# Kernel optimization log

Hardware: AMD Instinct MI355X
Metric: run time of the kernel (lower is better)

Reference implementation:

```python
import jax, jax.numpy as jnp
import numpy as np

COS_EPS = 1e-8
LN_EPS = 1e-5
N_HEADS = 8


def _merge(tokens, num_merge, wa, wb):
    """Faithful port of the torch merging loops.

    Torch computes topk(sim, num_merge) but the loop only reads indices[i,0]
    and indices[i,1] for i < num_merge, i.e. the top-2 per row -> we compute
    top_k(sim, 2) which yields identical values (modulo tie order).
    The per-step gather/average/scatter is sequential (later steps see earlier
    writes), so it is expressed as a lax.scan.
    """
    if num_merge == 0:
        return tokens
    n = jnp.linalg.norm(tokens, axis=-1)                      # [N]
    sim = (tokens @ tokens.T) / jnp.maximum(n[:, None] * n[None, :], COS_EPS)
    _, idx = jax.lax.top_k(sim, 2)                            # [N, 2]
    ab = idx[:num_merge]                                      # [num_merge, 2]

    def step(tok, ab_i):
        a, b = ab_i[0], ab_i[1]
        new = wa * tok[a] + wb * tok[b]
        # torch: tokens[a] = wa*tokens[a] + wb*tokens[b]; tokens[b] = tokens[a]
        return tok.at[a].set(new).at[b].set(new), None

    tokens, _ = jax.lax.scan(step, tokens, ab)
    return tokens[: tokens.shape[0] - num_merge]


def _layernorm(x, g, b):
    m = jnp.mean(x, axis=-1, keepdims=True)
    v = jnp.var(x, axis=-1, keepdims=True)
    return (x - m) * jax.lax.rsqrt(v + LN_EPS) * g + b


def _mha(x, Wqkv, bqkv, Wo, bo):
    """torch.nn.MultiheadAttention on an unbatched (L, D) input, q=k=v=x."""
    L, D = x.shape
    dh = D // N_HEADS
    qkv = x @ Wqkv.T + bqkv                                   # [L, 3D]
    q, k, v = jnp.split(qkv, 3, axis=-1)
    q = q.reshape(L, N_HEADS, dh)
    k = k.reshape(L, N_HEADS, dh)
    v = v.reshape(L, N_HEADS, dh)
    scores = jnp.einsum('qhd,khd->hqk', q, k) / np.float32(np.sqrt(dh))
    attn = jax.nn.softmax(scores, axis=-1)
    out = jnp.einsum('hqk,khd->qhd', attn, v).reshape(L, D)
    return out @ Wo.T + bo


def setup_inputs() -> dict:
    key = jax.random.key(0)
    ks = jax.random.split(key, 6)
    D = 768
    s = np.float32(0.02)
    return {
        'video_features': jax.random.normal(ks[0], (160, 50, D), jnp.float32),
        'Wqkv': jax.random.normal(ks[1], (3 * D, D), jnp.float32) * s,
        'bqkv': jnp.zeros((3 * D,), jnp.float32),
        'Wo': jax.random.normal(ks[2], (D, D), jnp.float32) * s,
        'bo': jnp.zeros((D,), jnp.float32),
        'ln1_g': jnp.ones((D,), jnp.float32),
        'ln1_b': jnp.zeros((D,), jnp.float32),
        'W1': jax.random.normal(ks[3], (4 * D, D), jnp.float32) * s,
        'b1': jnp.zeros((4 * D,), jnp.float32),
        'W2': jax.random.normal(ks[4], (D, 4 * D), jnp.float32) * s,
        'b2': jnp.zeros((D,), jnp.float32),
        'ln2_g': jnp.ones((D,), jnp.float32),
        'ln2_b': jnp.zeros((D,), jnp.float32),
    }


def reference(video_features, Wqkv, bqkv, Wo, bo, ln1_g, ln1_b,
              W1, b1, W2, b2, ln2_g, ln2_b):
    r = 0.5
    D = video_features.shape[-1]
    tokens = video_features.reshape(-1, D)                      # [8000, 768]
    tokens = _merge(tokens, int(tokens.shape[0] * r), 0.5, 0.5)       # img_me_block -> 4000
    tokens = _merge(tokens, int(tokens.shape[0] * r), 0.5, 0.5)       # cross_clip  -> 2000
    attn_out = _mha(tokens, Wqkv, bqkv, Wo, bo)
    tokens = _layernorm(tokens + attn_out, ln1_g, ln1_b)
    tokens = _merge(tokens, int(tokens.shape[0] * (r / 2)), 0.6, 0.4)  # intra_clip -> 1500
    ffn = jax.nn.gelu(tokens @ W1.T + b1, approximate=False) @ W2.T + b2
    return _layernorm(tokens + ffn, ln2_g, ln2_b)               # [1500, 768]
```

## Files before the change

### kernel.cpp

```cpp
#include <hip/hip_runtime.h>
#include <math.h>

#define D 768

__device__ __forceinline__ void dot4(float& acc, const float4& a, const float4& b) {
  acc += a.x * b.x; acc += a.y * b.y; acc += a.z * b.z; acc += a.w * b.w;
}

__global__ __launch_bounds__(256) void copy_f4(const float4* __restrict__ in,
                                               float4* __restrict__ out, int n) {
  int i = blockIdx.x * blockDim.x + threadIdx.x;
  if (i < n) out[i] = in[i];
}

__global__ __launch_bounds__(64) void norms_k(const float* __restrict__ tok,
                                              float* __restrict__ norms, int N) {
  int row = blockIdx.x;
  if (row >= N) return;
  const float* r = tok + (size_t)row * D;
  float s = 0.f;
  for (int k = threadIdx.x; k < D; k += 64) { float v = r[k]; s += v * v; }
#pragma unroll
  for (int off = 32; off > 0; off >>= 1) s += __shfl_down(s, off);
  if (threadIdx.x == 0) norms[row] = sqrtf(s);
}

__global__ __launch_bounds__(256) void sim_top2_v2(
    const float* __restrict__ tok, const float* __restrict__ norms,
    int nRows, int nCols, int nChunks, float4* __restrict__ part) {
  __shared__ float As[64][36];
  __shared__ float Bs[64][36];
  __shared__ float Ss[64][68];
  int tid = threadIdx.x;
  int rowBase = blockIdx.y * 64, colBase = blockIdx.x * 64;
  int tx = tid & 15, ty = tid >> 4;
  float acc[4][4] = {};
  int sr = tid >> 3, sc = (tid & 7) * 4;
  for (int kb = 0; kb < D; kb += 32) {
#pragma unroll
    for (int p = 0; p < 2; p++) {
      int r = sr + 32 * p;
      int ga = rowBase + r;
      float4 v = (ga < nRows) ? *(const float4*)&tok[(size_t)ga * D + kb + sc]
                              : make_float4(0.f, 0.f, 0.f, 0.f);
      *(float4*)&As[r][sc] = v;
      int gb = colBase + r;
      float4 w = (gb < nCols) ? *(const float4*)&tok[(size_t)gb * D + kb + sc]
                              : make_float4(0.f, 0.f, 0.f, 0.f);
      *(float4*)&Bs[r][sc] = w;
    }
    __syncthreads();
#pragma unroll
    for (int d = 0; d < 32; d += 4) {
      float4 a0 = *(float4*)&As[ty][d];
      float4 a1 = *(float4*)&As[ty + 16][d];
      float4 a2 = *(float4*)&As[ty + 32][d];
      float4 a3 = *(float4*)&As[ty + 48][d];
      float4 b0 = *(float4*)&Bs[tx][d];
      float4 b1 = *(float4*)&Bs[tx + 16][d];
      float4 b2 = *(float4*)&Bs[tx + 32][d];
      float4 b3 = *(float4*)&Bs[tx + 48][d];
      dot4(acc[0][0], a0, b0); dot4(acc[0][1], a0, b1); dot4(acc[0][2], a0, b2); dot4(acc[0][3], a0, b3);
      dot4(acc[1][0], a1, b0); dot4(acc[1][1], a1, b1); dot4(acc[1][2], a1, b2); dot4(acc[1][3], a1, b3);
      dot4(acc[2][0], a2, b0); dot4(acc[2][1], a2, b1); dot4(acc[2][2], a2, b2); dot4(acc[2][3], a2, b3);
      dot4(acc[3][0], a3, b0); dot4(acc[3][1], a3, b1); dot4(acc[3][2], a3, b2); dot4(acc[3][3], a3, b3);
    }
    __syncthreads();
  }
  float na[4], nc[4];
#pragma unroll
  for (int i = 0; i < 4; i++) { int r = rowBase + ty + 16 * i; na[i] = (r < nRows) ? norms[r] : 1.f; }
#pragma unroll
  for (int j = 0; j < 4; j++) { int c = colBase + tx + 16 * j; nc[j] = (c < nCols) ? norms[c] : 1.f; }
#pragma unroll
  for (int i = 0; i < 4; i++)
#pragma unroll
    for (int j = 0; j < 4; j++) {
      int c = colBase + tx + 16 * j;
      Ss[ty + 16 * i][tx + 16 * j] =
          (c < nCols) ? acc[i][j] / fmaxf(na[i] * nc[j], 1e-8f) : -INFINITY;
    }
  __syncthreads();
  if (tid < 64) {
    int row = rowBase + tid;
    if (row < nRows) {
      float v1 = -INFINITY, v2 = -INFINITY;
      int i1 = -1, i2 = -1;
      for (int c = 0; c < 64; c++) {
        float v = Ss[tid][c];
        int id = colBase + c;
        if (v > v1) { v2 = v1; i2 = i1; v1 = v; i1 = id; }
        else if (v > v2) { v2 = v; i2 = id; }
      }
      part[(size_t)row * nChunks + blockIdx.x] =
          make_float4(v1, __int_as_float(i1), v2, __int_as_float(i2));
    }
  }
}

__global__ __launch_bounds__(256) void top2_reduce(const float4* __restrict__ part,
                                                   int nRows, int nChunks,
                                                   int2* __restrict__ pairs) {
  int row = blockIdx.x * 256 + threadIdx.x;
  if (row >= nRows) return;
  float v1 = -INFINITY, v2 = -INFINITY;
  int i1 = -1, i2 = -1;
  for (int c = 0; c < nChunks; c++) {
    float4 p = part[(size_t)row * nChunks + c];
    float v = p.x; int id = __float_as_int(p.y);
    if (id >= 0) {
      if (v > v1) { v2 = v1; i2 = i1; v1 = v; i1 = id; }
      else if (v > v2) { v2 = v; i2 = id; }
    }
    v = p.z; id = __float_as_int(p.w);
    if (id >= 0) {
      if (v > v1) { v2 = v1; i2 = i1; v1 = v; i1 = id; }
      else if (v > v2) { v2 = v; i2 = id; }
    }
  }
  pairs[row] = make_int2(i1, i2);
}

#define MSG 8
__global__ __launch_bounds__(64) void merge_scan5(float* __restrict__ tok,
                                                  const int2* __restrict__ pairs,
                                                  int nm, float wa, float wb) {
  __shared__ int2 sp[4000];
  int t = blockIdx.x * 64 + threadIdx.x;
  for (int i = threadIdx.x; i < nm; i += 64) sp[i] = pairs[i];
  __syncthreads();
  int s = 0;
  for (; s + MSG <= nm; s += MSG) {
    int aa[MSG], bb[MSG];
    float xx[MSG], yy[MSG], vv[MSG];
#pragma unroll
    for (int c = 0; c < MSG; c++) {
      int2 p = sp[s + c]; aa[c] = p.x; bb[c] = p.y;
    }
#pragma unroll
    for (int c = 0; c < MSG; c++) {
      xx[c] = tok[(size_t)aa[c] * D + t];
      yy[c] = tok[(size_t)bb[c] * D + t];
    }
#pragma unroll
    for (int c = 0; c < MSG; c++) {
      float xv = xx[c], yv = yy[c];
#pragma unroll
      for (int j = 0; j < c; j++) {
        bool fa = (aa[c] == aa[j]) || (aa[c] == bb[j]);
        bool fb = (bb[c] == aa[j]) || (bb[c] == bb[j]);
        xv = fa ? vv[j] : xv;
        yv = fb ? vv[j] : yv;
      }
      vv[c] = wa * xv + wb * yv;
    }
#pragma unroll
    for (int c = 0; c < MSG; c++) {
      bool la = true, lb = true;
#pragma unroll
      for (int j = c + 1; j < MSG; j++) {
        la = la && (aa[j] != aa[c]) && (bb[j] != aa[c]);
        lb = lb && (aa[j] != bb[c]) && (bb[j] != bb[c]);
      }
      if (la) tok[(size_t)aa[c] * D + t] = vv[c];
      if (lb) tok[(size_t)bb[c] * D + t] = vv[c];
    }
  }
  for (; s < nm; s++) {
    int2 p = sp[s];
    float x = tok[(size_t)p.x * D + t];
    float y = tok[(size_t)p.y * D + t];
    float v = wa * x + wb * y;
    tok[(size_t)p.x * D + t] = v;
    tok[(size_t)p.y * D + t] = v;
  }
}

__global__ __launch_bounds__(256) void gemm_nt_v2(const float* __restrict__ A,
                                                  const float* __restrict__ B,
                                                  const float* __restrict__ bias,
                                                  float* __restrict__ C,
                                                  int M, int N, int K, int act) {
  __shared__ float As[64][36];
  __shared__ float Bs[64][36];
  int tid = threadIdx.x;
  int rowBase = blockIdx.y * 64, colBase = blockIdx.x * 64;
  int tx = tid & 15, ty = tid >> 4;
  float acc[4][4] = {};
  int sr = tid >> 3, sc = (tid & 7) * 4;
  for (int kb = 0; kb < K; kb += 32) {
#pragma unroll
    for (int p = 0; p < 2; p++) {
      int r = sr + 32 * p;
      int ga = rowBase + r;
      float4 v = (ga < M) ? *(const float4*)&A[(size_t)ga * K + kb + sc]
                          : make_float4(0.f, 0.f, 0.f, 0.f);
      *(float4*)&As[r][sc] = v;
      int gb = colBase + r;
      float4 w = (gb < N) ? *(const float4*)&B[(size_t)gb * K + kb + sc]
                          : make_float4(0.f, 0.f, 0.f, 0.f);
      *(float4*)&Bs[r][sc] = w;
    }
    __syncthreads();
#pragma unroll
    for (int d = 0; d < 32; d += 4) {
      float4 a0 = *(float4*)&As[ty][d];
      float4 a1 = *(float4*)&As[ty + 16][d];
      float4 a2 = *(float4*)&As[ty + 32][d];
      float4 a3 = *(float4*)&As[ty + 48][d];
      float4 b0 = *(float4*)&Bs[tx][d];
      float4 b1 = *(float4*)&Bs[tx + 16][d];
      float4 b2 = *(float4*)&Bs[tx + 32][d];
      float4 b3 = *(float4*)&Bs[tx + 48][d];
      dot4(acc[0][0], a0, b0); dot4(acc[0][1], a0, b1); dot4(acc[0][2], a0, b2); dot4(acc[0][3], a0, b3);
      dot4(acc[1][0], a1, b0); dot4(acc[1][1], a1, b1); dot4(acc[1][2], a1, b2); dot4(acc[1][3], a1, b3);
      dot4(acc[2][0], a2, b0); dot4(acc[2][1], a2, b1); dot4(acc[2][2], a2, b2); dot4(acc[2][3], a2, b3);
      dot4(acc[3][0], a3, b0); dot4(acc[3][1], a3, b1); dot4(acc[3][2], a3, b2); dot4(acc[3][3], a3, b3);
    }
    __syncthreads();
  }
#pragma unroll
  for (int i = 0; i < 4; i++)
#pragma unroll
    for (int j = 0; j < 4; j++) {
      int row = rowBase + ty + 16 * i, col = colBase + tx + 16 * j;
      if (row < M && col < N) {
        float v = acc[i][j] + bias[col];
        if (act == 1) v = 0.5f * v * (1.0f + erff(v * 0.70710678118654752f));
        C[(size_t)row * N + col] = v;
      }
    }
}

#define QT5 16
__global__ __launch_bounds__(512) void attn_k5(const float* __restrict__ qkv,
                                               float* __restrict__ attnb, int L) {
  int h = blockIdx.y;
  int q0 = blockIdx.x * QT5;
  __shared__ float qs[QT5][100];
  __shared__ float ks[64][100];
  __shared__ float vs[64][100];
  __shared__ float ss[QT5][68];
  __shared__ float mrow[QT5], lrow[QT5], corr[QT5];
  int tid = threadIdx.x;
  const float scale = 0.10206207261596577f;
  if (tid < QT5 * 24) {
    int i = tid / 24, c4 = (tid % 24) * 4;
    int qr = q0 + i;
    float4 v = (qr < L) ? *(const float4*)&qkv[(size_t)qr * 2304 + h * 96 + c4]
                        : make_float4(0.f, 0.f, 0.f, 0.f);
    *(float4*)&qs[i][c4] = v;
  }
  if (tid < QT5) { mrow[tid] = -INFINITY; lrow[tid] = 0.f; }
  int pi = tid / 24, gpd = tid % 24;
  bool pvact = tid < QT5 * 24;
  float oa0 = 0.f, oa1 = 0.f, oa2 = 0.f, oa3 = 0.f;
  __syncthreads();
  for (int c0 = 0; c0 < L; c0 += 64) {
    int cn = min(64, L - c0);
    for (int p = tid; p < 64 * 24; p += 512) {
      int r = p / 24, gc = p % 24;
      int pc = 4 * (gc ^ ((r >> 3) & 3));
      bool ok = r < cn;
      float4 kv4 = ok ? *(const float4*)&qkv[(size_t)(c0 + r) * 2304 + 768 + h * 96 + gc * 4]
                      : make_float4(0.f, 0.f, 0.f, 0.f);
      *(float4*)&ks[r][pc] = kv4;
      float4 vv4 = ok ? *(const float4*)&qkv[(size_t)(c0 + r) * 2304 + 1536 + h * 96 + gc * 4]
                      : make_float4(0.f, 0.f, 0.f, 0.f);
      *(float4*)&vs[r][pc] = vv4;
    }
    __syncthreads();
    {
      int qi = tid >> 5;
      int m = tid & 31;
      int swzm = (m >> 3) & 3;
      float a0 = 0.f, a1 = 0.f;
#pragma unroll
      for (int gd = 0; gd < 24; gd++) {
        float4 q4 = *(float4*)&qs[qi][4 * gd];
        int pc = 4 * (gd ^ swzm);
        float4 k0 = *(float4*)&ks[m][pc];
        float4 k1 = *(float4*)&ks[m + 32][pc];
        dot4(a0, q4, k0);
        dot4(a1, q4, k1);
      }
      ss[qi][m] = a0 * scale;
      ss[qi][m + 32] = a1 * scale;
    }
    __syncthreads();
    if (tid < QT5) {
      int i = tid;
      float m = mrow[i];
      float cm = -INFINITY;
      float sum = 0.f;
      if (cn == 64) {
#pragma unroll
        for (int j = 0; j < 64; j++) cm = fmaxf(cm, ss[i][j]);
        float nm = fmaxf(m, cm);
        float cr = expf(m - nm);
#pragma unroll
        for (int j = 0; j < 64; j++) { float p = expf(ss[i][j] - nm); ss[i][j] = p; sum += p; }
        lrow[i] = lrow[i] * cr + sum;
        mrow[i] = nm;
        corr[i] = cr;
      } else {
        for (int j = 0; j < cn; j++) cm = fmaxf(cm, ss[i][j]);
        float nm = fmaxf(m, cm);
        float cr = expf(m - nm);
        for (int j = 0; j < cn; j++) { float p = expf(ss[i][j] - nm); ss[i][j] = p; sum += p; }
        lrow[i] = lrow[i] * cr + sum;
        mrow[i] = nm;
        corr[i] = cr;
      }
    }
    __syncthreads();
    if (pvact) {
      float cr = corr[pi];
      oa0 *= cr; oa1 *= cr; oa2 *= cr; oa3 *= cr;
      if (cn == 64) {
#pragma unroll
        for (int jg = 0; jg < 16; jg++) {
          int j = 4 * jg;
          float4 s4 = *(float4*)&ss[pi][j];
          int pc = 4 * (gpd ^ ((jg >> 1) & 3));
          float4 v0 = *(float4*)&vs[j + 0][pc];
          float4 v1 = *(float4*)&vs[j + 1][pc];
          float4 v2 = *(float4*)&vs[j + 2][pc];
          float4 v3 = *(float4*)&vs[j + 3][pc];
          oa0 += s4.x * v0.x; oa1 += s4.x * v0.y; oa2 += s4.x * v0.z; oa3 += s4.x * v0.w;
          oa0 += s4.y * v1.x; oa1 += s4.y * v1.y; oa2 += s4.y * v1.z; oa3 += s4.y * v1.w;
          oa0 += s4.z * v2.x; oa1 += s4.z * v2.y; oa2 += s4.z * v2.z; oa3 += s4.z * v2.w;
          oa0 += s4.w * v3.x; oa1 += s4.w * v3.y; oa2 += s4.w * v3.z; oa3 += s4.w * v3.w;
        }
      } else {
        for (int j = 0; j < cn; j++) {
          float s = ss[pi][j];
          float4 vv = *(float4*)&vs[j][4 * (gpd ^ ((j >> 3) & 3))];
          oa0 += s * vv.x; oa1 += s * vv.y; oa2 += s * vv.z; oa3 += s * vv.w;
        }
      }
    }
    __syncthreads();
  }
  if (pvact) {
    int qr = q0 + pi;
    if (qr < L) {
      float li = lrow[pi];
      float4 o = make_float4(oa0 / li, oa1 / li, oa2 / li, oa3 / li);
      *(float4*)&attnb[(size_t)qr * D + h * 96 + gpd * 4] = o;
    }
  }
}

__global__ __launch_bounds__(256) void res_ln(const float* __restrict__ x,
                                              const float* __restrict__ r,
                                              const float* __restrict__ g,
                                              const float* __restrict__ b,
                                              float* __restrict__ out, int M) {
  int row = blockIdx.x;
  if (row >= M) return;
  __shared__ float buf[D];
  __shared__ float wred[4];
  __shared__ float stats[2];
  int tid = threadIdx.x;
  float s = 0.f;
  for (int k = tid; k < D; k += 256) {
    float v = x[(size_t)row * D + k] + r[(size_t)row * D + k];
    buf[k] = v;
    s += v;
  }
#pragma unroll
  for (int off = 32; off > 0; off >>= 1) s += __shfl_down(s, off);
  if ((tid & 63) == 0) wred[tid >> 6] = s;
  __syncthreads();
  if (tid == 0) stats[0] = (wred[0] + wred[1] + wred[2] + wred[3]) * (1.0f / D);
  __syncthreads();
  float mean = stats[0];
  float s2 = 0.f;
  for (int k = tid; k < D; k += 256) { float d0 = buf[k] - mean; s2 += d0 * d0; }
#pragma unroll
  for (int off = 32; off > 0; off >>= 1) s2 += __shfl_down(s2, off);
  __syncthreads();
  if ((tid & 63) == 0) wred[tid >> 6] = s2;
  __syncthreads();
  if (tid == 0)
    stats[1] = rsqrtf((wred[0] + wred[1] + wred[2] + wred[3]) * (1.0f / D) + 1e-5f);
  __syncthreads();
  float rstd = stats[1];
  for (int k = tid; k < D; k += 256)
    out[(size_t)row * D + k] = (buf[k] - mean) * rstd * g[k] + b[k];
}

extern "C" void kernel_launch(void* const* d_in, const int* in_sizes, int n_in,
                              void* d_out, int out_size, void* d_ws, size_t ws_size,
                              hipStream_t stream) {
  (void)in_sizes; (void)n_in; (void)out_size; (void)ws_size;
  const float* vf   = (const float*)d_in[0];
  const float* Wqkv = (const float*)d_in[1];
  const float* bqkv = (const float*)d_in[2];
  const float* Wo   = (const float*)d_in[3];
  const float* bo   = (const float*)d_in[4];
  const float* ln1g = (const float*)d_in[5];
  const float* ln1b = (const float*)d_in[6];
  const float* W1   = (const float*)d_in[7];
  const float* b1   = (const float*)d_in[8];
  const float* W2   = (const float*)d_in[9];
  const float* b2   = (const float*)d_in[10];
  const float* ln2g = (const float*)d_in[11];
  const float* ln2b = (const float*)d_in[12];

  float* ws = (float*)d_ws;
  float*  tok   = ws;
  float*  norms = ws + 6144000;
  float4* part  = (float4*)(ws + 6152000);
  int2*   pairs = (int2*)(ws + 8152000);
  float*  qkv   = ws + 8160000;
  float*  attnb = ws + 12768000;
  float*  projb = ws + 8160000;
  float*  hid   = ws + 8160000;
  float*  ffnb  = ws + 12768000;
  float*  outp  = (float*)d_out;

  copy_f4<<<6000, 256, 0, stream>>>((const float4*)vf, (float4*)tok, 1536000);

  norms_k<<<8000, 64, 0, stream>>>(tok, norms, 8000);
  sim_top2_v2<<<dim3(125, 63), 256, 0, stream>>>(tok, norms, 4000, 8000, 125, part);
  top2_reduce<<<(4000 + 255) / 256, 256, 0, stream>>>(part, 4000, 125, pairs);
  merge_scan5<<<12, 64, 0, stream>>>(tok, pairs, 4000, 0.5f, 0.5f);

  norms_k<<<4000, 64, 0, stream>>>(tok, norms, 4000);
  sim_top2_v2<<<dim3(63, 32), 256, 0, stream>>>(tok, norms, 2000, 4000, 63, part);
  top2_reduce<<<(2000 + 255) / 256, 256, 0, stream>>>(part, 2000, 63, pairs);
  merge_scan5<<<12, 64, 0, stream>>>(tok, pairs, 2000, 0.5f, 0.5f);

  gemm_nt_v2<<<dim3(36, 32), 256, 0, stream>>>(tok, Wqkv, bqkv, qkv, 2000, 2304, 768, 0);
  attn_k5<<<dim3(2000 / QT5, 8), 512, 0, stream>>>(qkv, attnb, 2000);
  gemm_nt_v2<<<dim3(12, 32), 256, 0, stream>>>(attnb, Wo, bo, projb, 2000, 768, 768, 0);
  res_ln<<<2000, 256, 0, stream>>>(tok, projb, ln1g, ln1b, tok, 2000);

  norms_k<<<2000, 64, 0, stream>>>(tok, norms, 2000);
  sim_top2_v2<<<dim3(32, 8), 256, 0, stream>>>(tok, norms, 500, 2000, 32, part);
  top2_reduce<<<(500 + 255) / 256, 256, 0, stream>>>(part, 500, 32, pairs);
  merge_scan5<<<12, 64, 0, stream>>>(tok, pairs, 500, 0.6f, 0.4f);

  gemm_nt_v2<<<dim3(48, 24), 256, 0, stream>>>(tok, W1, b1, hid, 1500, 3072, 768, 1);
  gemm_nt_v2<<<dim3(12, 24), 256, 0, stream>>>(hid, W2, b2, ffnb, 1500, 768, 3072, 0);
  res_ln<<<1500, 256, 0, stream>>>(tok, ffnb, ln2g, ln2b, outp, 1500);
}
```

Before: 4.217 ms.

## Schedule token merges by dependency level and evaluate independent steps in batches

Replaces the strictly sequential merge scan with two kernels. The first assigns each merge step a dependency level (one plus the latest level of either touched row), buckets steps by level and pads each bucket to a multiple of 16 with dummy row pairs. The second evaluates the levels in order, issuing 16 independent gather/average/scatter steps at a time, so loads overlap instead of forming a serial global-memory chain. It adds a single-thread level-assignment pass and dummy writes into scratch rows, and relies on the workspace regions that are reused not being live during the merge.

```diff
diff --git a/kernel.cpp b/kernel.cpp
--- a/kernel.cpp
+++ b/kernel.cpp
@@ -121,58 +121,119 @@
   pairs[row] = make_int2(i1, i2);
 }
 
-#define MSG 8
-__global__ __launch_bounds__(64) void merge_scan5(float* __restrict__ tok,
-                                                  const int2* __restrict__ pairs,
-                                                  int nm, float wa, float wb) {
-  __shared__ int2 sp[4000];
+#define MAXSTEPS 4000
+#define MAXROWS  8000
+__global__ __launch_bounds__(768) void merge_levels(
+    const int2* __restrict__ pairs, int nm, int2* __restrict__ opairs,
+    unsigned* __restrict__ lvlEnd, int* __restrict__ maxLevOut) {
+  __shared__ short sLast[MAXROWS];
+  __shared__ short sLev[MAXSTEPS];
+  __shared__ unsigned sCnt[MAXSTEPS + 1];
+  __shared__ unsigned sPair[MAXSTEPS];
+  __shared__ int sMaxLev;
+  int tid = threadIdx.x;
+  for (int i = tid; i < MAXROWS; i += 768) sLast[i] = 0;
+  for (int i = tid; i <= nm; i += 768) sCnt[i] = 0;
+  for (int i = tid; i < nm; i += 768) {
+    int2 p = pairs[i];
+    sPair[i] = (unsigned)p.x | ((unsigned)p.y << 16);
+  }
+  if (tid == 0) sMaxLev = 0;
+  __syncthreads();
+  if (tid == 0) {
+    int aP[3], bP[3], laP[3], lbP[3];
+#pragma unroll
+    for (int p = 0; p < 3; p++) {
+      if (p < nm) { unsigned pp = sPair[p]; aP[p] = (int)(pp & 0xffffu); bP[p] = (int)(pp >> 16); }
+      else { aP[p] = -1; bP[p] = -1; }
+      laP[p] = 0; lbP[p] = 0;
+    }
+    int h1a = -1, h1b = -1, h1L = 0, h2a = -1, h2b = -1, h2L = 0;
+    int maxLev = 0;
+    for (int i = 0; i < nm; i++) {
+      int sl = i % 3;
+      int a = aP[sl], b = bP[sl];
+      int la = laP[sl], lb = lbP[sl];
+      if (a == h1a || a == h1b) la = h1L;
+      else if (a == h2a || a == h2b) la = h2L;
+      if (b == h1a || b == h1b) lb = h1L;
+      else if (b == h2a || b == h2b) lb = h2L;
+      int L = (la > lb ? la : lb) + 1;
+      sLast[a] = (short)L;
+      sLast[b] = (short)L;
+      sLev[i] = (short)L;
+      if (L > maxLev) maxLev = L;
+      h2a = h1a; h2b = h1b; h2L = h1L;
+      h1a = a; h1b = b; h1L = L;
+      int nx = i + 3;
+      if (nx < nm) {
+        unsigned pp = sPair[nx];
+        int na_ = (int)(pp & 0xffffu), nb_ = (int)(pp >> 16);
+        aP[sl] = na_; bP[sl] = nb_;
+        laP[sl] = sLast[na_];
+        lbP[sl] = sLast[nb_];
+      }
+    }
+    sMaxLev = maxLev;
+  }
+  __syncthreads();
+  int maxLev = sMaxLev;
+  if (tid == 0) *maxLevOut = maxLev;
+  for (int i = tid; i < nm; i += 768) atomicAdd(&sCnt[(int)sLev[i]], 1u);
+  __syncthreads();
+  if (tid == 0) {
+    unsigned run = 0;
+    for (int l = 1; l <= maxLev; l++) {
+      unsigned c = sCnt[l];
+      sCnt[l] = run;
+      run += (c + 15u) & ~15u;
+      lvlEnd[l] = run;
+    }
+  }
+  __syncthreads();
+  for (int i = tid; i < nm; i += 768) {
+    int l = (int)sLev[i];
+    unsigned pos = atomicAdd(&sCnt[l], 1u);
+    unsigned pp = sPair[i];
+    opairs[pos] = make_int2((int)(pp & 0xffffu), (int)(pp >> 16));
+  }
+  __syncthreads();
+  for (int l = 1 + tid; l <= maxLev; l += 768) {
+    unsigned fillTo = lvlEnd[l];
+    for (unsigned p = sCnt[l]; p < fillTo; p++) {
+      int d = (int)(p & 15u);
+      opairs[p] = make_int2(16000 + 2 * d, 16001 + 2 * d);
+    }
+  }
+}
+
+__global__ __launch_bounds__(64) void merge_eval(
+    float* __restrict__ tok, const int2* __restrict__ opairs,
+    const unsigned* __restrict__ lvlEnd, const int* __restrict__ maxLevPtr,
+    float wa, float wb) {
   int t = blockIdx.x * 64 + threadIdx.x;
-  for (int i = threadIdx.x; i < nm; i += 64) sp[i] = pairs[i];
-  __syncthreads();
-  int s = 0;
-  for (; s + MSG <= nm; s += MSG) {
-    int aa[MSG], bb[MSG];
-    float xx[MSG], yy[MSG], vv[MSG];
-#pragma unroll
-    for (int c = 0; c < MSG; c++) {
-      int2 p = sp[s + c]; aa[c] = p.x; bb[c] = p.y;
-    }
-#pragma unroll
-    for (int c = 0; c < MSG; c++) {
-      xx[c] = tok[(size_t)aa[c] * D + t];
-      yy[c] = tok[(size_t)bb[c] * D + t];
-    }
-#pragma unroll
-    for (int c = 0; c < MSG; c++) {
-      float xv = xx[c], yv = yy[c];
-#pragma unroll
-      for (int j = 0; j < c; j++) {
-        bool fa = (aa[c] == aa[j]) || (aa[c] == bb[j]);
-        bool fb = (bb[c] == aa[j]) || (bb[c] == bb[j]);
-        xv = fa ? vv[j] : xv;
-        yv = fb ? vv[j] : yv;
-      }
-      vv[c] = wa * xv + wb * yv;
-    }
-#pragma unroll
-    for (int c = 0; c < MSG; c++) {
-      bool la = true, lb = true;
-#pragma unroll
-      for (int j = c + 1; j < MSG; j++) {
-        la = la && (aa[j] != aa[c]) && (bb[j] != aa[c]);
-        lb = lb && (aa[j] != bb[c]) && (bb[j] != bb[c]);
-      }
-      if (la) tok[(size_t)aa[c] * D + t] = vv[c];
-      if (lb) tok[(size_t)bb[c] * D + t] = vv[c];
-    }
-  }
-  for (; s < nm; s++) {
-    int2 p = sp[s];
-    float x = tok[(size_t)p.x * D + t];
-    float y = tok[(size_t)p.y * D + t];
-    float v = wa * x + wb * y;
-    tok[(size_t)p.x * D + t] = v;
-    tok[(size_t)p.y * D + t] = v;
+  int maxLev = *maxLevPtr;
+  unsigned begin = 0;
+  for (int l = 1; l <= maxLev; l++) {
+    unsigned end = lvlEnd[l];
+    for (unsigned s = begin; s < end; s += 16) {
+      int2 pr[16];
+      float xv[16], yv[16];
+#pragma unroll
+      for (int c = 0; c < 16; c++) pr[c] = opairs[s + c];
+#pragma unroll
+      for (int c = 0; c < 16; c++) {
+        xv[c] = tok[(size_t)pr[c].x * D + t];
+        yv[c] = tok[(size_t)pr[c].y * D + t];
+      }
+#pragma unroll
+      for (int c = 0; c < 16; c++) {
+        float v = wa * xv[c] + wb * yv[c];
+        tok[(size_t)pr[c].x * D + t] = v;
+        tok[(size_t)pr[c].y * D + t] = v;
+      }
+    }
+    begin = end;
   }
 }
 
@@ -410,28 +471,33 @@
   const float* ln2b = (const float*)d_in[12];
 
   float* ws = (float*)d_ws;
-  float*  tok   = ws;
-  float*  norms = ws + 6144000;
-  float4* part  = (float4*)(ws + 6152000);
-  int2*   pairs = (int2*)(ws + 8152000);
-  float*  qkv   = ws + 8160000;
-  float*  attnb = ws + 12768000;
-  float*  projb = ws + 8160000;
-  float*  hid   = ws + 8160000;
-  float*  ffnb  = ws + 12768000;
-  float*  outp  = (float*)d_out;
+  float*    tok     = ws;
+  float*    norms   = ws + 6144000;
+  int2*     opairs  = (int2*)(ws + 6152000);
+  unsigned* lvlEnd  = (unsigned*)(ws + 6400000);
+  int*      maxLevP = (int*)(ws + 6410000);
+  float4*   part    = (float4*)(ws + 6152000);
+  int2*     pairs   = (int2*)(ws + 8152000);
+  float*    qkv     = ws + 8160000;
+  float*    attnb   = ws + 12768000;
+  float*    projb   = ws + 8160000;
+  float*    hid     = ws + 8160000;
+  float*    ffnb    = ws + 12768000;
+  float*    outp    = (float*)d_out;
 
   copy_f4<<<6000, 256, 0, stream>>>((const float4*)vf, (float4*)tok, 1536000);
 
   norms_k<<<8000, 64, 0, stream>>>(tok, norms, 8000);
   sim_top2_v2<<<dim3(125, 63), 256, 0, stream>>>(tok, norms, 4000, 8000, 125, part);
   top2_reduce<<<(4000 + 255) / 256, 256, 0, stream>>>(part, 4000, 125, pairs);
-  merge_scan5<<<12, 64, 0, stream>>>(tok, pairs, 4000, 0.5f, 0.5f);
+  merge_levels<<<1, 768, 0, stream>>>(pairs, 4000, opairs, lvlEnd, maxLevP);
+  merge_eval<<<12, 64, 0, stream>>>(tok, opairs, lvlEnd, maxLevP, 0.5f, 0.5f);
 
   norms_k<<<4000, 64, 0, stream>>>(tok, norms, 4000);
   sim_top2_v2<<<dim3(63, 32), 256, 0, stream>>>(tok, norms, 2000, 4000, 63, part);
   top2_reduce<<<(2000 + 255) / 256, 256, 0, stream>>>(part, 2000, 63, pairs);
-  merge_scan5<<<12, 64, 0, stream>>>(tok, pairs, 2000, 0.5f, 0.5f);
+  merge_levels<<<1, 768, 0, stream>>>(pairs, 2000, opairs, lvlEnd, maxLevP);
+  merge_eval<<<12, 64, 0, stream>>>(tok, opairs, lvlEnd, maxLevP, 0.5f, 0.5f);
 
   gemm_nt_v2<<<dim3(36, 32), 256, 0, stream>>>(tok, Wqkv, bqkv, qkv, 2000, 2304, 768, 0);
   attn_k5<<<dim3(2000 / QT5, 8), 512, 0, stream>>>(qkv, attnb, 2000);
@@ -441,7 +507,8 @@
   norms_k<<<2000, 64, 0, stream>>>(tok, norms, 2000);
   sim_top2_v2<<<dim3(32, 8), 256, 0, stream>>>(tok, norms, 500, 2000, 32, part);
   top2_reduce<<<(500 + 255) / 256, 256, 0, stream>>>(part, 500, 32, pairs);
-  merge_scan5<<<12, 64, 0, stream>>>(tok, pairs, 500, 0.6f, 0.4f);
+  merge_levels<<<1, 768, 0, stream>>>(pairs, 500, opairs, lvlEnd, maxLevP);
+  merge_eval<<<12, 64, 0, stream>>>(tok, opairs, lvlEnd, maxLevP, 0.6f, 0.4f);
 
   gemm_nt_v2<<<dim3(48, 24), 256, 0, stream>>>(tok, W1, b1, hid, 1500, 3072, 768, 1);
   gemm_nt_v2<<<dim3(12, 24), 256, 0, stream>>>(hid, W2, b2, ffnb, 1500, 768, 3072, 0);
```

Measured after the change: 4.771 ms. 1.13x slower.
